# Kernel optimization log

Hardware: AMD Instinct MI355X
Metric: run time of the kernel (lower is better)

## Reference

```python
import jax, jax.numpy as jnp
import numpy as np

EMBED_DIM = 1024
SCALE = 1.0 / float(np.sqrt(EMBED_DIM))


def setup_inputs() -> dict:
    key = jax.random.key(0)
    ks = jax.random.split(key, 9)
    B, S, D = 4, 4096, EMBED_DIM
    std = 1.0 / float(np.sqrt(D))
    x = jax.random.normal(ks[0], (B, S, D), dtype=jnp.float32)
    Wq = jax.random.normal(ks[1], (D, D), dtype=jnp.float32) * std
    Wk = jax.random.normal(ks[2], (D, D), dtype=jnp.float32) * std
    Wv = jax.random.normal(ks[3], (D, D), dtype=jnp.float32) * std
    Wo = jax.random.normal(ks[4], (D, D), dtype=jnp.float32) * std
    bq = jax.random.normal(ks[5], (D,), dtype=jnp.float32) * std
    bk = jax.random.normal(ks[6], (D,), dtype=jnp.float32) * std
    bv = jax.random.normal(ks[7], (D,), dtype=jnp.float32) * std
    bo = jax.random.normal(ks[8], (D,), dtype=jnp.float32) * std
    return {"x": x, "Wq": Wq, "bq": bq, "Wk": Wk, "bk": bk,
            "Wv": Wv, "bv": bv, "Wo": Wo, "bo": bo}


def reference(x, Wq, bq, Wk, bk, Wv, bv, Wo, bo):
    # q/k/v projections: x @ W^T + b (torch Linear convention: W is [out, in])
    q = jnp.einsum('bsd,ed->bse', x, Wq) + bq
    k = jnp.einsum('bsd,ed->bse', x, Wk) + bk
    v = jnp.einsum('bsd,ed->bse', x, Wv) + bv
    # naive attention: full [B, S, S] scores, softmax over keys
    scores = jnp.einsum('bqd,bkd->bqk', q, k) * SCALE
    attn = jax.nn.softmax(scores, axis=-1)
    context = jnp.einsum('bqk,bkd->bqd', attn, v)
    out = jnp.einsum('bsd,ed->bse', context, Wo) + bo
    return out
```

## Files before the change

kernel.cpp:

```cpp
#include <hip/hip_runtime.h>
#include <stdint.h>

#define BATCH 4
#define S_LEN 4096
#define D_DIM 1024
static constexpr float ATTN_SCALE = 0.03125f;

typedef __attribute__((ext_vector_type(8))) short short8_t;
typedef __attribute__((ext_vector_type(4))) float f32x4;

__device__ __forceinline__ unsigned short f2b(float f) {
    union { float f; uint32_t i; } x; x.f = f;
    uint32_t r = x.i + 0x7FFF + ((x.i >> 16) & 1);
    return (unsigned short)(r >> 16);
}
__device__ __forceinline__ float b2f(unsigned short u) {
    union { uint32_t i; float f; } x; x.i = ((uint32_t)u) << 16;
    return x.f;
}

__device__ __forceinline__ void gl_lds16(const unsigned short* g, unsigned short* l) {
    __builtin_amdgcn_global_load_lds(
        (const __attribute__((address_space(1))) uint32_t*)(const void*)g,
        (__attribute__((address_space(3))) uint32_t*)(void*)l,
        16, 0, 0);
}

__global__ __launch_bounds__(256) void cast_f32_bf16(
    const float* __restrict__ in, unsigned short* __restrict__ out, int n) {
    int i = (blockIdx.x * 256 + threadIdx.x) * 8;
    if (i >= n) return;
    float4 a = *(const float4*)(in + i);
    float4 b = *(const float4*)(in + i + 4);
    short8_t o;
    o[0] = (short)f2b(a.x); o[1] = (short)f2b(a.y);
    o[2] = (short)f2b(a.z); o[3] = (short)f2b(a.w);
    o[4] = (short)f2b(b.x); o[5] = (short)f2b(b.y);
    o[6] = (short)f2b(b.z); o[7] = (short)f2b(b.w);
    *(short8_t*)(out + i) = o;
}

__global__ __launch_bounds__(256) void pack_bias(
    const float* __restrict__ bq, const float* __restrict__ bk,
    const float* __restrict__ bv, float* __restrict__ o) {
    int i = blockIdx.x * 256 + threadIdx.x;
    float v = (i < 1024) ? bq[i] : (i < 2048 ? bk[i - 1024] : bv[i - 2048]);
    o[i] = v;
}

__device__ __forceinline__ void storeC(float* p, float v) { *p = v; }
__device__ __forceinline__ void storeC(unsigned short* p, float v) { *p = f2b(v); }

template <typename OutT>
__global__ __launch_bounds__(256) void gemm_bt(
    const unsigned short* __restrict__ A, const unsigned short* __restrict__ B,
    OutT* __restrict__ C, const float* __restrict__ bias,
    int M, int N, int K, int lda, int ldb, int ldc,
    size_t sA, size_t sB, size_t sC, float scale) {
    __shared__ __align__(16) unsigned short As[128 * 32];
    __shared__ __align__(16) unsigned short Bs[128 * 32];

    A += (size_t)blockIdx.z * sA;
    B += (size_t)blockIdx.z * sB;
    C += (size_t)blockIdx.z * sC;

    const int tid  = threadIdx.x;
    const int wave = tid >> 6;
    const int lane = tid & 63;
    const int m0 = blockIdx.y * 128;
    const int n0 = blockIdx.x * 128;
    const int wm = (wave >> 1) * 64;
    const int wn = (wave & 1) * 64;
    const int lm = lane & 15;
    const int quad = lane >> 4;

    f32x4 acc[4][4];
#pragma unroll
    for (int i = 0; i < 4; ++i)
#pragma unroll
        for (int j = 0; j < 4; ++j)
#pragma unroll
            for (int e = 0; e < 4; ++e) acc[i][j][e] = 0.f;

    const int c0 = tid, c1 = tid + 256;
    const int r0 = c0 >> 2, kc0 = (c0 & 3) << 3;
    const int r1 = c1 >> 2, kc1 = (c1 & 3) << 3;
    const unsigned short* Ar0 = A + (size_t)(m0 + r0) * lda + kc0;
    const unsigned short* Ar1 = A + (size_t)(m0 + r1) * lda + kc1;
    const unsigned short* Br0 = B + (size_t)(n0 + r0) * ldb + kc0;
    const unsigned short* Br1 = B + (size_t)(n0 + r1) * ldb + kc1;

    for (int k0 = 0; k0 < K; k0 += 32) {
        gl_lds16(Ar0 + k0, &As[c0 * 8]);
        gl_lds16(Ar1 + k0, &As[c1 * 8]);
        gl_lds16(Br0 + k0, &Bs[c0 * 8]);
        gl_lds16(Br1 + k0, &Bs[c1 * 8]);
        __syncthreads();

        short8_t af[4], bf[4];
#pragma unroll
        for (int mi = 0; mi < 4; ++mi)
            af[mi] = *(const short8_t*)&As[(wm + mi * 16 + lm) * 32 + quad * 8];
#pragma unroll
        for (int ni = 0; ni < 4; ++ni)
            bf[ni] = *(const short8_t*)&Bs[(wn + ni * 16 + lm) * 32 + quad * 8];
#pragma unroll
        for (int mi = 0; mi < 4; ++mi)
#pragma unroll
            for (int ni = 0; ni < 4; ++ni)
                acc[mi][ni] = __builtin_amdgcn_mfma_f32_16x16x32_bf16(
                    af[mi], bf[ni], acc[mi][ni], 0, 0, 0);
        __syncthreads();
    }

#pragma unroll
    for (int ni = 0; ni < 4; ++ni) {
        const int col = n0 + wn + ni * 16 + lm;
        const float bv = bias ? bias[col] : 0.f;
#pragma unroll
        for (int mi = 0; mi < 4; ++mi) {
#pragma unroll
            for (int e = 0; e < 4; ++e) {
                const int row = m0 + wm + mi * 16 + quad * 4 + e;
                storeC(&C[(size_t)row * ldc + col], acc[mi][ni][e] * scale + bv);
            }
        }
    }
}

__global__ __launch_bounds__(256) void softmax_rows(unsigned short* __restrict__ P) {
    const int row = blockIdx.x;
    unsigned short* p = P + (size_t)row * S_LEN;
    const int t = threadIdx.x;

    short8_t r0 = ((const short8_t*)p)[2 * t];
    short8_t r1 = ((const short8_t*)p)[2 * t + 1];
    float v[16];
    float m = -1e30f;
#pragma unroll
    for (int i = 0; i < 8; ++i) { v[i] = b2f((unsigned short)r0[i]); m = fmaxf(m, v[i]); }
#pragma unroll
    for (int i = 0; i < 8; ++i) { v[8 + i] = b2f((unsigned short)r1[i]); m = fmaxf(m, v[8 + i]); }

#pragma unroll
    for (int off = 32; off >= 1; off >>= 1) m = fmaxf(m, __shfl_xor(m, off));
    __shared__ float redm[4];
    if ((t & 63) == 0) redm[t >> 6] = m;
    __syncthreads();
    m = fmaxf(fmaxf(redm[0], redm[1]), fmaxf(redm[2], redm[3]));

    float s = 0.f;
#pragma unroll
    for (int i = 0; i < 16; ++i) { v[i] = __expf(v[i] - m); s += v[i]; }
#pragma unroll
    for (int off = 32; off >= 1; off >>= 1) s += __shfl_xor(s, off);
    __shared__ float reds[4];
    if ((t & 63) == 0) reds[t >> 6] = s;
    __syncthreads();
    s = reds[0] + reds[1] + reds[2] + reds[3];
    const float inv = 1.f / s;

    short8_t w0, w1;
#pragma unroll
    for (int i = 0; i < 8; ++i) w0[i] = (short)f2b(v[i] * inv);
#pragma unroll
    for (int i = 0; i < 8; ++i) w1[i] = (short)f2b(v[8 + i] * inv);
    ((short8_t*)p)[2 * t] = w0;
    ((short8_t*)p)[2 * t + 1] = w1;
}

__global__ __launch_bounds__(256) void transpose_sd(
    const unsigned short* __restrict__ src, int srcLd, size_t sSrc,
    unsigned short* __restrict__ dst, size_t sDst) {
    __shared__ unsigned short tile[32][33];
    src += (size_t)blockIdx.z * sSrc;
    dst += (size_t)blockIdx.z * sDst;
    const int d = blockIdx.x * 32 + threadIdx.x;
    const int s = blockIdx.y * 32 + threadIdx.y;
#pragma unroll
    for (int j = 0; j < 32; j += 8)
        tile[threadIdx.y + j][threadIdx.x] = src[(size_t)(s + j) * srcLd + d];
    __syncthreads();
    const int d2 = blockIdx.x * 32 + threadIdx.y;
    const int s2 = blockIdx.y * 32 + threadIdx.x;
#pragma unroll
    for (int j = 0; j < 32; j += 8)
        dst[(size_t)(d2 + j) * S_LEN + s2] = tile[threadIdx.x][threadIdx.y + j];
}

extern "C" void kernel_launch(void* const* d_in, const int* in_sizes, int n_in,
                              void* d_out, int out_size, void* d_ws, size_t ws_size,
                              hipStream_t stream) {
    const float* x  = (const float*)d_in[0];
    const float* Wq = (const float*)d_in[1];
    const float* bq = (const float*)d_in[2];
    const float* Wk = (const float*)d_in[3];
    const float* bk = (const float*)d_in[4];
    const float* Wv = (const float*)d_in[5];
    const float* bv = (const float*)d_in[6];
    const float* Wo = (const float*)d_in[7];
    const float* bo = (const float*)d_in[8];
    float* out = (float*)d_out;

    char* ws = (char*)d_ws;
    const size_t MB = 1ull << 20;
    const int nX = BATCH * S_LEN * D_DIM;
    const int nW = D_DIM * D_DIM;
    const int SR = BATCH * S_LEN;

    int nb = 0;
    if (ws_size >= 169 * MB + 32 * MB)
        nb = (int)((ws_size - 169 * MB) / (32 * MB));
    if (nb > BATCH) nb = BATCH;

    if (nb >= 1) {
        unsigned short* qkvb  = (unsigned short*)(ws + 0);
        unsigned short* Wqkvb = (unsigned short*)(ws + 96 * MB);
        unsigned short* Wob   = (unsigned short*)(ws + 102 * MB);
        float*          bqkv  = (float*)(ws + 104 * MB);
        unsigned short* xb    = (unsigned short*)(ws + 105 * MB);
        unsigned short* vtb   = (unsigned short*)(ws + 105 * MB);
        unsigned short* ctx   = (unsigned short*)(ws + 137 * MB);
        unsigned short* Pb    = (unsigned short*)(ws + 169 * MB);

        cast_f32_bf16<<<nX / 2048, 256, 0, stream>>>(x, xb, nX);
        cast_f32_bf16<<<nW / 2048, 256, 0, stream>>>(Wq, Wqkvb, nW);
        cast_f32_bf16<<<nW / 2048, 256, 0, stream>>>(Wk, Wqkvb + nW, nW);
        cast_f32_bf16<<<nW / 2048, 256, 0, stream>>>(Wv, Wqkvb + 2 * nW, nW);
        cast_f32_bf16<<<nW / 2048, 256, 0, stream>>>(Wo, Wob, nW);
        pack_bias<<<12, 256, 0, stream>>>(bq, bk, bv, bqkv);

        gemm_bt<unsigned short><<<dim3(3072 / 128, SR / 128, 1), 256, 0, stream>>>(
            xb, Wqkvb, qkvb, bqkv, SR, 3072, D_DIM,
            D_DIM, D_DIM, 3072, 0, 0, 0, 1.f);

        transpose_sd<<<dim3(D_DIM / 32, S_LEN / 32, BATCH), dim3(32, 8), 0, stream>>>(
            qkvb + 2048, 3072, (size_t)S_LEN * 3072, vtb, (size_t)D_DIM * S_LEN);

        const unsigned short* qp = qkvb;
        const unsigned short* kp = qkvb + 1024;
        for (int b0 = 0; b0 < BATCH; b0 += nb) {
            int g = (BATCH - b0 < nb) ? (BATCH - b0) : nb;
            const size_t qoff = (size_t)b0 * S_LEN * 3072;
            gemm_bt<unsigned short><<<dim3(S_LEN / 128, S_LEN / 128, g), 256, 0, stream>>>(
                qp + qoff, kp + qoff, Pb, nullptr, S_LEN, S_LEN, D_DIM,
                3072, 3072, S_LEN,
                (size_t)S_LEN * 3072, (size_t)S_LEN * 3072, (size_t)S_LEN * S_LEN,
                ATTN_SCALE);
            softmax_rows<<<g * S_LEN, 256, 0, stream>>>(Pb);
            gemm_bt<unsigned short><<<dim3(D_DIM / 128, S_LEN / 128, g), 256, 0, stream>>>(
                Pb, vtb + (size_t)b0 * D_DIM * S_LEN,
                ctx + (size_t)b0 * S_LEN * D_DIM, nullptr,
                S_LEN, D_DIM, S_LEN,
                S_LEN, S_LEN, D_DIM,
                (size_t)S_LEN * S_LEN, (size_t)D_DIM * S_LEN, (size_t)S_LEN * D_DIM,
                1.f);
        }

        gemm_bt<float><<<dim3(D_DIM / 128, SR / 128, 1), 256, 0, stream>>>(
            ctx, Wob, out, bo, SR, D_DIM, D_DIM,
            D_DIM, D_DIM, D_DIM, 0, 0, 0, 1.f);
    } else {
        unsigned short* xb  = (unsigned short*)(ws + 0);
        unsigned short* Pb  = (unsigned short*)(ws + 0);
        unsigned short* Wqb = (unsigned short*)(ws + 32 * MB);
        unsigned short* Wkb = (unsigned short*)(ws + 34 * MB);
        unsigned short* Wvb = (unsigned short*)(ws + 36 * MB);
        unsigned short* Wob = (unsigned short*)(ws + 38 * MB);
        unsigned short* qb  = (unsigned short*)(ws + 40 * MB);
        unsigned short* kb  = (unsigned short*)(ws + 72 * MB);
        unsigned short* vb  = (unsigned short*)(ws + 104 * MB);
        unsigned short* vtb = (unsigned short*)(ws + 136 * MB);
        unsigned short* ctx = (unsigned short*)(ws + 168 * MB);

        cast_f32_bf16<<<nX / 2048, 256, 0, stream>>>(x, xb, nX);
        cast_f32_bf16<<<nW / 2048, 256, 0, stream>>>(Wq, Wqb, nW);
        cast_f32_bf16<<<nW / 2048, 256, 0, stream>>>(Wk, Wkb, nW);
        cast_f32_bf16<<<nW / 2048, 256, 0, stream>>>(Wv, Wvb, nW);
        cast_f32_bf16<<<nW / 2048, 256, 0, stream>>>(Wo, Wob, nW);

        dim3 gproj(D_DIM / 128, SR / 128, 1);
        gemm_bt<unsigned short><<<gproj, 256, 0, stream>>>(xb, Wqb, qb, bq,
            SR, D_DIM, D_DIM, D_DIM, D_DIM, D_DIM, 0, 0, 0, 1.f);
        gemm_bt<unsigned short><<<gproj, 256, 0, stream>>>(xb, Wkb, kb, bk,
            SR, D_DIM, D_DIM, D_DIM, D_DIM, D_DIM, 0, 0, 0, 1.f);
        gemm_bt<unsigned short><<<gproj, 256, 0, stream>>>(xb, Wvb, vb, bv,
            SR, D_DIM, D_DIM, D_DIM, D_DIM, D_DIM, 0, 0, 0, 1.f);

        transpose_sd<<<dim3(D_DIM / 32, S_LEN / 32, BATCH), dim3(32, 8), 0, stream>>>(
            vb, D_DIM, (size_t)S_LEN * D_DIM, vtb, (size_t)D_DIM * S_LEN);

        for (int b = 0; b < BATCH; ++b) {
            const size_t sd = (size_t)b * S_LEN * D_DIM;
            const size_t ds = (size_t)b * D_DIM * S_LEN;
            gemm_bt<unsigned short><<<dim3(S_LEN / 128, S_LEN / 128, 1), 256, 0, stream>>>(
                qb + sd, kb + sd, Pb, nullptr, S_LEN, S_LEN, D_DIM,
                D_DIM, D_DIM, S_LEN, 0, 0, 0, ATTN_SCALE);
            softmax_rows<<<S_LEN, 256, 0, stream>>>(Pb);
            gemm_bt<unsigned short><<<dim3(D_DIM / 128, S_LEN / 128, 1), 256, 0, stream>>>(
                Pb, vtb + ds, ctx, nullptr, S_LEN, D_DIM, S_LEN,
                S_LEN, S_LEN, D_DIM, 0, 0, 0, 1.f);
            gemm_bt<float><<<dim3(D_DIM / 128, S_LEN / 128, 1), 256, 0, stream>>>(
                ctx, Wob, out + sd, bo, S_LEN, D_DIM, D_DIM,
                D_DIM, D_DIM, D_DIM, 0, 0, 0, 1.f);
        }
    }
}
```

Measured before the change: 820.7 us.

## Fuse softmax into attention GEMM epilogues and write V transposed directly

Folds the exponentiation into the QK^T GEMM epilogue with atomically accumulated row sums, and applies the normalization in the PV GEMM epilogue, removing the separate softmax pass over the full score matrix. The QKV projection epilogue writes V already transposed, eliminating the transpose kernel, and all casts plus bias packing are merged into one prep kernel. The max subtraction is dropped, so large scores could overflow exp, and the atomics add some contention.

```diff
diff --git a/kernel.cpp b/kernel.cpp
--- a/kernel.cpp
+++ b/kernel.cpp
@@ -26,10 +26,7 @@
         16, 0, 0);
 }
 
-__global__ __launch_bounds__(256) void cast_f32_bf16(
-    const float* __restrict__ in, unsigned short* __restrict__ out, int n) {
-    int i = (blockIdx.x * 256 + threadIdx.x) * 8;
-    if (i >= n) return;
+__device__ __forceinline__ void cast8(const float* in, unsigned short* out, int i) {
     float4 a = *(const float4*)(in + i);
     float4 b = *(const float4*)(in + i + 4);
     short8_t o;
@@ -40,23 +37,49 @@
     *(short8_t*)(out + i) = o;
 }
 
-__global__ __launch_bounds__(256) void pack_bias(
+__global__ __launch_bounds__(256) void prep(
+    const float* __restrict__ x,
+    const float* __restrict__ Wq, const float* __restrict__ Wk,
+    const float* __restrict__ Wv, const float* __restrict__ Wo,
     const float* __restrict__ bq, const float* __restrict__ bk,
-    const float* __restrict__ bv, float* __restrict__ o) {
-    int i = blockIdx.x * 256 + threadIdx.x;
-    float v = (i < 1024) ? bq[i] : (i < 2048 ? bk[i - 1024] : bv[i - 2048]);
-    o[i] = v;
+    const float* __restrict__ bv,
+    unsigned short* __restrict__ xb, unsigned short* __restrict__ Wqkvb,
+    unsigned short* __restrict__ Wob, float* __restrict__ bqkv) {
+    const int nX8 = (BATCH * S_LEN * D_DIM) / 8;
+    const int nW8 = (D_DIM * D_DIM) / 8;
+    int gid = blockIdx.x * 256 + threadIdx.x;
+    if (gid < nX8) { cast8(x, xb, gid * 8); return; }
+    gid -= nX8;
+    if (gid < nW8) { cast8(Wq, Wqkvb, gid * 8); return; }
+    gid -= nW8;
+    if (gid < nW8) { cast8(Wk, Wqkvb + D_DIM * D_DIM, gid * 8); return; }
+    gid -= nW8;
+    if (gid < nW8) { cast8(Wv, Wqkvb + 2 * D_DIM * D_DIM, gid * 8); return; }
+    gid -= nW8;
+    if (gid < nW8) { cast8(Wo, Wob, gid * 8); return; }
+    gid -= nW8;
+    if (gid < 384) {
+        int i = gid * 8;
+#pragma unroll
+        for (int e = 0; e < 8; ++e) {
+            int j = i + e;
+            bqkv[j] = (j < 1024) ? bq[j] : (j < 2048 ? bk[j - 1024] : bv[j - 2048]);
+        }
+    }
 }
 
 __device__ __forceinline__ void storeC(float* p, float v) { *p = v; }
 __device__ __forceinline__ void storeC(unsigned short* p, float v) { *p = f2b(v); }
 
-template <typename OutT>
+enum { EPI_STORE = 0, EPI_QKV = 1, EPI_EXP = 2, EPI_INV = 3 };
+
+template <typename OutT, int EPI>
 __global__ __launch_bounds__(256) void gemm_bt(
     const unsigned short* __restrict__ A, const unsigned short* __restrict__ B,
     OutT* __restrict__ C, const float* __restrict__ bias,
     int M, int N, int K, int lda, int ldb, int ldc,
-    size_t sA, size_t sB, size_t sC, float scale) {
+    size_t sA, size_t sB, size_t sC, float scale,
+    float* __restrict__ rs, unsigned short* __restrict__ vt) {
     __shared__ __align__(16) unsigned short As[128 * 32];
     __shared__ __align__(16) unsigned short Bs[128 * 32];
 
@@ -113,17 +136,105 @@
         __syncthreads();
     }
 
-#pragma unroll
-    for (int ni = 0; ni < 4; ++ni) {
-        const int col = n0 + wn + ni * 16 + lm;
-        const float bv = bias ? bias[col] : 0.f;
+    if (EPI == EPI_STORE) {
+#pragma unroll
+        for (int ni = 0; ni < 4; ++ni) {
+            const int col = n0 + wn + ni * 16 + lm;
+            const float bv = bias ? bias[col] : 0.f;
+#pragma unroll
+            for (int mi = 0; mi < 4; ++mi)
+#pragma unroll
+                for (int e = 0; e < 4; ++e) {
+                    const int row = m0 + wm + mi * 16 + quad * 4 + e;
+                    storeC(&C[(size_t)row * ldc + col], acc[mi][ni][e] * scale + bv);
+                }
+        }
+    } else if (EPI == EPI_QKV) {
+        if (n0 < 2048) {
+#pragma unroll
+            for (int ni = 0; ni < 4; ++ni) {
+                const int col = n0 + wn + ni * 16 + lm;
+                const float bv = bias[col];
+#pragma unroll
+                for (int mi = 0; mi < 4; ++mi)
+#pragma unroll
+                    for (int e = 0; e < 4; ++e) {
+                        const int row = m0 + wm + mi * 16 + quad * 4 + e;
+                        storeC(&C[(size_t)row * ldc + col], acc[mi][ni][e] + bv);
+                    }
+            }
+        } else {
+#pragma unroll
+            for (int ni = 0; ni < 4; ++ni) {
+                const int col = n0 + wn + ni * 16 + lm;
+                const int d = col - 2048;
+                const float bv = bias[col];
+#pragma unroll
+                for (int mi = 0; mi < 4; ++mi) {
+                    const int rr = m0 + wm + mi * 16 + quad * 4;
+                    const int b = rr >> 12, s0 = rr & 4095;
+                    ushort4 w;
+                    w.x = f2b(acc[mi][ni][0] + bv);
+                    w.y = f2b(acc[mi][ni][1] + bv);
+                    w.z = f2b(acc[mi][ni][2] + bv);
+                    w.w = f2b(acc[mi][ni][3] + bv);
+                    *(ushort4*)&vt[((size_t)(b * D_DIM + d)) * S_LEN + s0] = w;
+                }
+            }
+        }
+    } else if (EPI == EPI_EXP) {
+        float rp[4][4];
+#pragma unroll
+        for (int mi = 0; mi < 4; ++mi)
+#pragma unroll
+            for (int e = 0; e < 4; ++e) rp[mi][e] = 0.f;
+#pragma unroll
+        for (int ni = 0; ni < 4; ++ni) {
+            const int col = n0 + wn + ni * 16 + lm;
+#pragma unroll
+            for (int mi = 0; mi < 4; ++mi)
+#pragma unroll
+                for (int e = 0; e < 4; ++e) {
+                    const int row = m0 + wm + mi * 16 + quad * 4 + e;
+                    const float p = __expf(acc[mi][ni][e] * scale);
+                    storeC(&C[(size_t)row * ldc + col], p);
+                    rp[mi][e] += p;
+                }
+        }
+#pragma unroll
+        for (int off = 1; off <= 8; off <<= 1)
+#pragma unroll
+            for (int mi = 0; mi < 4; ++mi)
+#pragma unroll
+                for (int e = 0; e < 4; ++e)
+                    rp[mi][e] += __shfl_xor(rp[mi][e], off);
+        if (lm == 0) {
+            float* rsz = rs + (size_t)blockIdx.z * M;
+#pragma unroll
+            for (int mi = 0; mi < 4; ++mi)
+#pragma unroll
+                for (int e = 0; e < 4; ++e)
+                    atomicAdd(&rsz[m0 + wm + mi * 16 + quad * 4 + e], rp[mi][e]);
+        }
+    } else {
+        const float* rsz = rs + (size_t)blockIdx.z * M;
+        float inv[4][4];
 #pragma unroll
         for (int mi = 0; mi < 4; ++mi) {
-#pragma unroll
-            for (int e = 0; e < 4; ++e) {
-                const int row = m0 + wm + mi * 16 + quad * 4 + e;
-                storeC(&C[(size_t)row * ldc + col], acc[mi][ni][e] * scale + bv);
-            }
+            float4 s4 = *(const float4*)&rsz[m0 + wm + mi * 16 + quad * 4];
+            inv[mi][0] = 1.f / s4.x; inv[mi][1] = 1.f / s4.y;
+            inv[mi][2] = 1.f / s4.z; inv[mi][3] = 1.f / s4.w;
+        }
+#pragma unroll
+        for (int ni = 0; ni < 4; ++ni) {
+            const int col = n0 + wn + ni * 16 + lm;
+#pragma unroll
+            for (int mi = 0; mi < 4; ++mi)
+#pragma unroll
+                for (int e = 0; e < 4; ++e) {
+                    const int row = m0 + wm + mi * 16 + quad * 4 + e;
+                    storeC(&C[(size_t)row * ldc + col], acc[mi][ni][e] * inv[mi][e]);
+                }
         }
     }
 }
@@ -132,7 +243,6 @@
     const int row = blockIdx.x;
     unsigned short* p = P + (size_t)row * S_LEN;
     const int t = threadIdx.x;
-
     short8_t r0 = ((const short8_t*)p)[2 * t];
     short8_t r1 = ((const short8_t*)p)[2 * t + 1];
     float v[16];
@@ -141,14 +251,12 @@
     for (int i = 0; i < 8; ++i) { v[i] = b2f((unsigned short)r0[i]); m = fmaxf(m, v[i]); }
 #pragma unroll
     for (int i = 0; i < 8; ++i) { v[8 + i] = b2f((unsigned short)r1[i]); m = fmaxf(m, v[8 + i]); }
-
 #pragma unroll
     for (int off = 32; off >= 1; off >>= 1) m = fmaxf(m, __shfl_xor(m, off));
     __shared__ float redm[4];
     if ((t & 63) == 0) redm[t >> 6] = m;
     __syncthreads();
     m = fmaxf(fmaxf(redm[0], redm[1]), fmaxf(redm[2], redm[3]));
-
     float s = 0.f;
 #pragma unroll
     for (int i = 0; i < 16; ++i) { v[i] = __expf(v[i] - m); s += v[i]; }
@@ -159,7 +267,6 @@
     __syncthreads();
     s = reds[0] + reds[1] + reds[2] + reds[3];
     const float inv = 1.f / s;
-
     short8_t w0, w1;
 #pragma unroll
     for (int i = 0; i < 8; ++i) w0[i] = (short)f2b(v[i] * inv);
@@ -204,9 +311,11 @@
 
     char* ws = (char*)d_ws;
     const size_t MB = 1ull << 20;
+    const size_t KB = 1ull << 10;
     const int nX = BATCH * S_LEN * D_DIM;
     const int nW = D_DIM * D_DIM;
     const int SR = BATCH * S_LEN;
+    const int prepBlocks = (nX / 8 + 4 * (nW / 8) + 384 + 255) / 256;
 
     int nb = 0;
     if (ws_size >= 169 * MB + 32 * MB)
@@ -214,78 +323,68 @@
     if (nb > BATCH) nb = BATCH;
 
     if (nb >= 1) {
-        unsigned short* qkvb  = (unsigned short*)(ws + 0);
+        unsigned short* qkb   = (unsigned short*)(ws + 0);
+        unsigned short* vtb   = (unsigned short*)(ws + 64 * MB);
         unsigned short* Wqkvb = (unsigned short*)(ws + 96 * MB);
         unsigned short* Wob   = (unsigned short*)(ws + 102 * MB);
         float*          bqkv  = (float*)(ws + 104 * MB);
+        float*          rowS  = (float*)(ws + 104 * MB + 64 * KB);
         unsigned short* xb    = (unsigned short*)(ws + 105 * MB);
-        unsigned short* vtb   = (unsigned short*)(ws + 105 * MB);
         unsigned short* ctx   = (unsigned short*)(ws + 137 * MB);
         unsigned short* Pb    = (unsigned short*)(ws + 169 * MB);
 
-        cast_f32_bf16<<<nX / 2048, 256, 0, stream>>>(x, xb, nX);
-        cast_f32_bf16<<<nW / 2048, 256, 0, stream>>>(Wq, Wqkvb, nW);
-        cast_f32_bf16<<<nW / 2048, 256, 0, stream>>>(Wk, Wqkvb + nW, nW);
-        cast_f32_bf16<<<nW / 2048, 256, 0, stream>>>(Wv, Wqkvb + 2 * nW, nW);
-        cast_f32_bf16<<<nW / 2048, 256, 0, stream>>>(Wo, Wob, nW);
-        pack_bias<<<12, 256, 0, stream>>>(bq, bk, bv, bqkv);
-
-        gemm_bt<unsigned short><<<dim3(3072 / 128, SR / 128, 1), 256, 0, stream>>>(
-            xb, Wqkvb, qkvb, bqkv, SR, 3072, D_DIM,
-            D_DIM, D_DIM, 3072, 0, 0, 0, 1.f);
-
-        transpose_sd<<<dim3(D_DIM / 32, S_LEN / 32, BATCH), dim3(32, 8), 0, stream>>>(
-            qkvb + 2048, 3072, (size_t)S_LEN * 3072, vtb, (size_t)D_DIM * S_LEN);
-
-        const unsigned short* qp = qkvb;
-        const unsigned short* kp = qkvb + 1024;
+        hipMemsetAsync(rowS, 0, (size_t)SR * sizeof(float), stream);
+        prep<<<prepBlocks, 256, 0, stream>>>(x, Wq, Wk, Wv, Wo, bq, bk, bv,
+                                             xb, Wqkvb, Wob, bqkv);
+
+        gemm_bt<unsigned short, EPI_QKV><<<dim3(3072 / 128, SR / 128, 1), 256, 0, stream>>>(
+            xb, Wqkvb, qkb, bqkv, SR, 3072, D_DIM,
+            D_DIM, D_DIM, 2048, 0, 0, 0, 1.f, nullptr, vtb);
+
+        const unsigned short* qp = qkb;
+        const unsigned short* kp = qkb + 1024;
         for (int b0 = 0; b0 < BATCH; b0 += nb) {
             int g = (BATCH - b0 < nb) ? (BATCH - b0) : nb;
-            const size_t qoff = (size_t)b0 * S_LEN * 3072;
-            gemm_bt<unsigned short><<<dim3(S_LEN / 128, S_LEN / 128, g), 256, 0, stream>>>(
+            const size_t qoff = (size_t)b0 * S_LEN * 2048;
+            gemm_bt<unsigned short, EPI_EXP><<<dim3(S_LEN / 128, S_LEN / 128, g), 256, 0, stream>>>(
                 qp + qoff, kp + qoff, Pb, nullptr, S_LEN, S_LEN, D_DIM,
-                3072, 3072, S_LEN,
-                (size_t)S_LEN * 3072, (size_t)S_LEN * 3072, (size_t)S_LEN * S_LEN,
-                ATTN_SCALE);
-            softmax_rows<<<g * S_LEN, 256, 0, stream>>>(Pb);
-            gemm_bt<unsigned short><<<dim3(D_DIM / 128, S_LEN / 128, g), 256, 0, stream>>>(
+                2048, 2048, S_LEN,
+                (size_t)S_LEN * 2048, (size_t)S_LEN * 2048, (size_t)S_LEN * S_LEN,
+                ATTN_SCALE, rowS + (size_t)b0 * S_LEN, nullptr);
+            gemm_bt<unsigned short, EPI_INV><<<dim3(D_DIM / 128, S_LEN / 128, g), 256, 0, stream>>>(
                 Pb, vtb + (size_t)b0 * D_DIM * S_LEN,
                 ctx + (size_t)b0 * S_LEN * D_DIM, nullptr,
                 S_LEN, D_DIM, S_LEN,
                 S_LEN, S_LEN, D_DIM,
                 (size_t)S_LEN * S_LEN, (size_t)D_DIM * S_LEN, (size_t)S_LEN * D_DIM,
-                1.f);
-        }
-
-        gemm_bt<float><<<dim3(D_DIM / 128, SR / 128, 1), 256, 0, stream>>>(
+                1.f, rowS + (size_t)b0 * S_LEN, nullptr);
+        }
+
+        gemm_bt<float, EPI_STORE><<<dim3(D_DIM / 128, SR / 128, 1), 256, 0, stream>>>(
             ctx, Wob, out, bo, SR, D_DIM, D_DIM,
-            D_DIM, D_DIM, D_DIM, 0, 0, 0, 1.f);
+            D_DIM, D_DIM, D_DIM, 0, 0, 0, 1.f, nullptr, nullptr);
     } else {
-        unsigned short* xb  = (unsigned short*)(ws + 0);
-        unsigned short* Pb  = (unsigned short*)(ws + 0);
-        unsigned short* Wqb = (unsigned short*)(ws + 32 * MB);
-        unsigned short* Wkb = (unsigned short*)(ws + 34 * MB);
-        unsigned short* Wvb = (unsigned short*)(ws + 36 * MB);
-        unsigned short* Wob = (unsigned short*)(ws + 38 * MB);
-        unsigned short* qb  = (unsigned short*)(ws + 40 * MB);
-        unsigned short* kb  = (unsigned short*)(ws + 72 * MB);
-        unsigned short* vb  = (unsigned short*)(ws + 104 * MB);
-        unsigned short* vtb = (unsigned short*)(ws + 136 * MB);
-        unsigned short* ctx = (unsigned short*)(ws + 168 * MB);
-
-        cast_f32_bf16<<<nX / 2048, 256, 0, stream>>>(x, xb, nX);
-        cast_f32_bf16<<<nW / 2048, 256, 0, stream>>>(Wq, Wqb, nW);
-        cast_f32_bf16<<<nW / 2048, 256, 0, stream>>>(Wk, Wkb, nW);
-        cast_f32_bf16<<<nW / 2048, 256, 0, stream>>>(Wv, Wvb, nW);
-        cast_f32_bf16<<<nW / 2048, 256, 0, stream>>>(Wo, Wob, nW);
+        unsigned short* xb    = (unsigned short*)(ws + 0);
+        unsigned short* Pb    = (unsigned short*)(ws + 0);
+        unsigned short* Wqkvb = (unsigned short*)(ws + 32 * MB);
+        unsigned short* Wob   = (unsigned short*)(ws + 38 * MB);
+        float*          bqkv  = (float*)(ws + 40 * MB);
+        unsigned short* qb    = (unsigned short*)(ws + 41 * MB);
+        unsigned short* kb    = (unsigned short*)(ws + 73 * MB);
+        unsigned short* vb    = (unsigned short*)(ws + 105 * MB);
+        unsigned short* vtb   = (unsigned short*)(ws + 137 * MB);
+        unsigned short* ctx   = (unsigned short*)(ws + 169 * MB);
+
+        prep<<<prepBlocks, 256, 0, stream>>>(x, Wq, Wk, Wv, Wo, bq, bk, bv,
+                                             xb, Wqkvb, Wob, bqkv);
 
         dim3 gproj(D_DIM / 128, SR / 128, 1);
-        gemm_bt<unsigned short><<<gproj, 256, 0, stream>>>(xb, Wqb, qb, bq,
-            SR, D_DIM, D_DIM, D_DIM, D_DIM, D_DIM, 0, 0, 0, 1.f);
-        gemm_bt<unsigned short><<<gproj, 256, 0, stream>>>(xb, Wkb, kb, bk,
-            SR, D_DIM, D_DIM, D_DIM, D_DIM, D_DIM, 0, 0, 0, 1.f);
-        gemm_bt<unsigned short><<<gproj, 256, 0, stream>>>(xb, Wvb, vb, bv,
-            SR, D_DIM, D_DIM, D_DIM, D_DIM, D_DIM, 0, 0, 0, 1.f);
+        gemm_bt<unsigned short, EPI_STORE><<<gproj, 256, 0, stream>>>(xb, Wqkvb, qb, bq,
+            SR, D_DIM, D_DIM, D_DIM, D_DIM, D_DIM, 0, 0, 0, 1.f, nullptr, nullptr);
+        gemm_bt<unsigned short, EPI_STORE><<<gproj, 256, 0, stream>>>(xb, Wqkvb + nW, kb, bk,
+            SR, D_DIM, D_DIM, D_DIM, D_DIM, D_DIM, 0, 0, 0, 1.f, nullptr, nullptr);
+        gemm_bt<unsigned short, EPI_STORE><<<gproj, 256, 0, stream>>>(xb, Wqkvb + 2 * nW, vb, bv,
+            SR, D_DIM, D_DIM, D_DIM, D_DIM, D_DIM, 0, 0, 0, 1.f, nullptr, nullptr);
 
         transpose_sd<<<dim3(D_DIM / 32, S_LEN / 32, BATCH), dim3(32, 8), 0, stream>>>(
             vb, D_DIM, (size_t)S_LEN * D_DIM, vtb, (size_t)D_DIM * S_LEN);
@@ -293,16 +392,16 @@
         for (int b = 0; b < BATCH; ++b) {
             const size_t sd = (size_t)b * S_LEN * D_DIM;
             const size_t ds = (size_t)b * D_DIM * S_LEN;
-            gemm_bt<unsigned short><<<dim3(S_LEN / 128, S_LEN / 128, 1), 256, 0, stream>>>(
+            gemm_bt<unsigned short, EPI_STORE><<<dim3(S_LEN / 128, S_LEN / 128, 1), 256, 0, stream>>>(
                 qb + sd, kb + sd, Pb, nullptr, S_LEN, S_LEN, D_DIM,
-                D_DIM, D_DIM, S_LEN, 0, 0, 0, ATTN_SCALE);
+                D_DIM, D_DIM, S_LEN, 0, 0, 0, ATTN_SCALE, nullptr, nullptr);
             softmax_rows<<<S_LEN, 256, 0, stream>>>(Pb);
-            gemm_bt<unsigned short><<<dim3(D_DIM / 128, S_LEN / 128, 1), 256, 0, stream>>>(
+            gemm_bt<unsigned short, EPI_STORE><<<dim3(D_DIM / 128, S_LEN / 128, 1), 256, 0, stream>>>(
                 Pb, vtb + ds, ctx, nullptr, S_LEN, D_DIM, S_LEN,
-                S_LEN, S_LEN, D_DIM, 0, 0, 0, 1.f);
-            gemm_bt<float><<<dim3(D_DIM / 128, S_LEN / 128, 1), 256, 0, stream>>>(
+                S_LEN, S_LEN, D_DIM, 0, 0, 0, 1.f, nullptr, nullptr);
+            gemm_bt<float, EPI_STORE><<<dim3(D_DIM / 128, S_LEN / 128, 1), 256, 0, stream>>>(
                 ctx, Wob, out + sd, bo, S_LEN, D_DIM, D_DIM,
-                D_DIM, D_DIM, D_DIM, 0, 0, 0, 1.f);
+                D_DIM, D_DIM, D_DIM, 0, 0, 0, 1.f, nullptr, nullptr);
         }
     }
 }
```

Result: no change. 828.7 us (+1.0%).
